# Kernel optimization log

Hardware: AMD Instinct MI355X
Metric: run time of the kernel (lower is better)

Reference implementation:

```python
import jax, jax.numpy as jnp
import numpy as np
from jax import lax

D_MODEL = 512
D_INNER = 1024   # expand=2
D_STATE = 16
D_CONV = 4
DT_RANK = 32     # ceil(d_model/16)
B = 32
T_LOW = 512
T_SKIP = 1024    # = 2*T_LOW (convtranspose k=4,s=2,p=1 doubles T)


def setup_inputs() -> dict:
    key = jax.random.key(0)
    ks = jax.random.split(key, 12)
    def rn(k, shape, scale):
        return jax.random.normal(k, shape, jnp.float32) * scale
    d, di = D_MODEL, D_INNER
    return {
        "x": rn(ks[0], (B, T_LOW, d), 1.0),
        "skip": rn(ks[1], (B, T_SKIP, d), 1.0),
        # ConvTranspose1d weight, torch layout (in, out, k)
        "up_w": rn(ks[2], (d, d, 4), (d * 4) ** -0.5),
        "up_b": jnp.zeros((d,), jnp.float32),
        # 1x1 fusion conv: (out, in=2d)
        "fus_w": rn(ks[3], (d, 2 * d), (2 * d) ** -0.5),
        "fus_b": jnp.zeros((d,), jnp.float32),
        "ln_g": jnp.ones((d,), jnp.float32),
        "ln_b": jnp.zeros((d,), jnp.float32),
        # Mamba params (1 layer)
        "in_w": rn(ks[4], (2 * di, d), d ** -0.5),
        "conv_w": rn(ks[5], (di, 1, D_CONV), D_CONV ** -0.5),  # depthwise
        "conv_b": jnp.zeros((di,), jnp.float32),
        "xproj_w": rn(ks[6], (DT_RANK + 2 * D_STATE, di), di ** -0.5),
        "dt_w": rn(ks[7], (di, DT_RANK), DT_RANK ** -0.5),
        "dt_b": jnp.log(jnp.expm1(jax.random.uniform(ks[8], (di,), jnp.float32, 1e-3, 0.1))),
        "A_log": jnp.log(jnp.tile(jnp.arange(1, D_STATE + 1, dtype=jnp.float32), (di, 1))),
        "Dp": jnp.ones((di,), jnp.float32),
        "out_w": rn(ks[9], (d, di), di ** -0.5),
    }


def reference(x, skip, up_w, up_b, fus_w, fus_b, ln_g, ln_b,
              in_w, conv_w, conv_b, xproj_w, dt_w, dt_b, A_log, Dp, out_w):
    # --- upsample: ConvTranspose1d(k=4, s=2, p=1): (B,T_low,d) -> (B,d,2*T_low)
    xc = x.transpose(0, 2, 1)                                  # (B, d, T_low)
    wt = jnp.swapaxes(jnp.flip(up_w, -1), 0, 1)                # (out, in, k)
    xu = lax.conv_general_dilated(
        xc, wt, window_strides=(1,), padding=[(2, 2)], lhs_dilation=(2,),
        dimension_numbers=("NCH", "OIH", "NCH")) + up_b[None, :, None]
    # T_up == T_skip by construction (no interpolate/slice needed)

    # --- skip fusion: concat on channels, 1x1 conv
    fused = jnp.concatenate([xu, skip.transpose(0, 2, 1)], axis=1)  # (B, 2d, T)
    fused = jnp.einsum("bct,oc->bto", fused, fus_w) + fus_b         # (B, T, d)

    # --- LayerNorm over d_model
    mu = fused.mean(-1, keepdims=True)
    var = fused.var(-1, keepdims=True)
    h = (fused - mu) * lax.rsqrt(var + 1e-5) * ln_g + ln_b

    # --- Mamba layer (mamba_ssm defaults) ---
    xz = h @ in_w.T                                            # (B, T, 2*Din)
    x_in, z = jnp.split(xz, 2, axis=-1)
    # causal depthwise conv1d (torch pads d_conv-1 both sides then truncates)
    xch = x_in.transpose(0, 2, 1)                              # (B, Din, T)
    xconv = lax.conv_general_dilated(
        xch, conv_w, window_strides=(1,), padding=[(D_CONV - 1, 0)],
        feature_group_count=D_INNER,
        dimension_numbers=("NCH", "OIH", "NCH")) + conv_b[None, :, None]
    xs = jax.nn.silu(xconv.transpose(0, 2, 1))                 # (B, T, Din)

    x_dbl = xs @ xproj_w.T                                     # (B, T, dt_rank+2S)
    dtr, Bm, Cm = jnp.split(x_dbl, [DT_RANK, DT_RANK + D_STATE], axis=-1)
    dt = jax.nn.softplus(dtr @ dt_w.T + dt_b)                  # (B, T, Din)
    A = -jnp.exp(A_log)                                        # (Din, S)

    def step(hst, ins):
        dt_t, b_t, c_t, x_t = ins                              # (B,Din),(B,S),(B,S),(B,Din)
        da = jnp.exp(dt_t[..., None] * A)                      # (B, Din, S)
        hst = hst * da + (dt_t * x_t)[..., None] * b_t[:, None, :]
        y = jnp.einsum("bds,bs->bd", hst, c_t)
        return hst, y

    h0 = jnp.zeros((xs.shape[0], D_INNER, D_STATE), xs.dtype)
    _, ys = lax.scan(step, h0, (dt.transpose(1, 0, 2), Bm.transpose(1, 0, 2),
                                Cm.transpose(1, 0, 2), xs.transpose(1, 0, 2)))
    y = ys.transpose(1, 0, 2) + xs * Dp                        # (B, T, Din)
    y = y * jax.nn.silu(z)
    out = y @ out_w.T                                          # (B, T, d)
    # dropout is identity in eval mode
    return out
```

## Files before the change

### kernel.cpp

```cpp
#include <hip/hip_runtime.h>
#include <hip/hip_bf16.h>
#include <math.h>

#define Bn    32
#define TLOW  512
#define Tt    1024
#define Dm    512
#define Din   1024
#define Dst   16
#define DTR   32
#define NC    16
#define Tc    64
#define L2E   1.44269504f

typedef unsigned short ushortt;
typedef __bf16 bf16x8 __attribute__((ext_vector_type(8)));
typedef unsigned short u16x8 __attribute__((ext_vector_type(8)));
typedef unsigned short u16x4 __attribute__((ext_vector_type(4)));
typedef float  f32x4  __attribute__((ext_vector_type(4)));

__device__ __forceinline__ ushortt f2b(float f) {
  union { float f; unsigned int u; } v; v.f = f;
  unsigned int r = v.u + 0x7FFFu + ((v.u >> 16) & 1u);
  return (ushortt)(r >> 16);
}
__device__ __forceinline__ float b2f(ushortt h) {
  union { unsigned int u; float f; } v; v.u = ((unsigned int)h) << 16;
  return v.f;
}
__device__ __forceinline__ ushortt f2h(float f) {
  _Float16 h = (_Float16)f; ushortt u; __builtin_memcpy(&u, &h, 2); return u;
}
__device__ __forceinline__ float h2f(ushortt u) {
  _Float16 h; __builtin_memcpy(&h, &u, 2); return (float)h;
}
__device__ __forceinline__ void gload16(const ushortt* g, ushortt* l) {
  __builtin_amdgcn_global_load_lds(
      (const __attribute__((address_space(1))) unsigned int*)g,
      (__attribute__((address_space(3))) unsigned int*)l, 16, 0, 0);
}
__device__ __forceinline__ float softplusf(float v) {
  float e = __builtin_amdgcn_exp2f(-fabsf(v) * L2E);
  return fmaxf(v, 0.f) + __logf(1.f + e);
}

template <typename OUT_T>
__global__ __launch_bounds__(256) void gemm_bf16(
    const ushortt* __restrict__ A0, const ushortt* __restrict__ A1,
    int lda, int ksplit,
    const ushortt* __restrict__ W,
    const float* __restrict__ bias,
    OUT_T* __restrict__ C, int ldc,
    int M, int N, int K, int bpad, int zA1, int zW, int zC)
{
  const int z = blockIdx.z;
  A1 += (size_t)z * zA1;
  W  += (size_t)z * zW;
  C  += (size_t)z * zC;

  __shared__ ushortt smem[8192];
  ushortt* As = smem;
  ushortt* Ws = smem + 4096;
  const int tid = threadIdx.x;
  const int m0 = blockIdx.y * 128;
  const int n0 = blockIdx.x * 128;
  const int lane = tid & 63;
  const int wv = tid >> 6;
  const int wm = wv & 1, wn = wv >> 1;
  const int arow0 = m0 + (bpad ? 2 * (m0 >> 9) : 0);

  f32x4 zz; zz[0] = 0.f; zz[1] = 0.f; zz[2] = 0.f; zz[3] = 0.f;
  f32x4 acc[4][4];
#pragma unroll
  for (int i = 0; i < 4; ++i)
#pragma unroll
    for (int j = 0; j < 4; ++j) acc[i][j] = zz;

  const int s0 = tid, s1 = tid + 256;
  const int r0 = s0 >> 2, c0 = (s0 & 3) * 8;
  const int r1 = s1 >> 2, c1 = (s1 & 3) * 8;

  for (int k0 = 0; k0 < K; k0 += 32) {
    const ushortt* Ab; int kc;
    if (k0 < ksplit) { Ab = A0; kc = k0; } else { Ab = A1; kc = k0 - ksplit; }
    gload16(Ab + (size_t)(arow0 + r0) * lda + kc + c0, As + s0 * 8);
    gload16(Ab + (size_t)(arow0 + r1) * lda + kc + c1, As + s1 * 8);
    gload16(W + (size_t)(n0 + r0) * K + k0 + c0, Ws + s0 * 8);
    gload16(W + (size_t)(n0 + r1) * K + k0 + c1, Ws + s1 * 8);
    __syncthreads();

    bf16x8 af[4], bfr[4];
    const int kk = (lane >> 4) * 8;
    const int ar = wm * 64 + (lane & 15);
    const int br = wn * 64 + (lane & 15);
#pragma unroll
    for (int i = 0; i < 4; ++i)
      af[i] = *(const bf16x8*)(As + (ar + i * 16) * 32 + kk);
#pragma unroll
    for (int i = 0; i < 4; ++i)
      bfr[i] = *(const bf16x8*)(Ws + (br + i * 16) * 32 + kk);
#pragma unroll
    for (int i = 0; i < 4; ++i)
#pragma unroll
      for (int j = 0; j < 4; ++j)
        acc[i][j] = __builtin_amdgcn_mfma_f32_16x16x32_bf16(af[i], bfr[j], acc[i][j], 0, 0, 0);
    __syncthreads();
  }

  const int crow = (lane >> 4) * 4;
  const int ccol = lane & 15;
  float bv[4];
#pragma unroll
  for (int j = 0; j < 4; ++j)
    bv[j] = bias ? bias[n0 + wn * 64 + j * 16 + ccol] : 0.f;

  if constexpr (sizeof(OUT_T) == 2) {
    for (int ph = 0; ph < 2; ++ph) {
      __syncthreads();
      if (wm == ph) {
#pragma unroll
        for (int i = 0; i < 4; ++i) {
          const int rl = i * 16 + crow;
#pragma unroll
          for (int j = 0; j < 4; ++j) {
            const int cl = wn * 64 + j * 16 + ccol;
#pragma unroll
            for (int ii = 0; ii < 4; ++ii) {
              const int r = rl + ii;
              const int cs = cl ^ (((r >> 2) & 7) << 4);
              smem[r * 128 + cs] = f2b(acc[i][j][ii] + bv[j]);
            }
          }
        }
      }
      __syncthreads();
      const int grb = m0 + ph * 64;
#pragma unroll
      for (int q = 0; q < 4; ++q) {
        const int g = tid + q * 256;
        const int r = g >> 4;
        const int cg = (g & 15) * 8;
        const int cs = cg ^ (((r >> 2) & 7) << 4);
        u16x8 v = *(const u16x8*)(smem + r * 128 + cs);
        *(u16x8*)((ushortt*)C + (size_t)(grb + r) * ldc + n0 + cg) = v;
      }
    }
  } else {
    float* smf = (float*)smem;
    for (int ph = 0; ph < 4; ++ph) {
      __syncthreads();
      if (wm == (ph >> 1)) {
#pragma unroll
        for (int io = 0; io < 2; ++io) {
          const int i = (ph & 1) * 2 + io;
          const int rl = i * 16 + crow - (ph & 1) * 32;
#pragma unroll
          for (int j = 0; j < 4; ++j) {
            const int cl = wn * 64 + j * 16 + ccol;
#pragma unroll
            for (int ii = 0; ii < 4; ++ii) {
              const int r = rl + ii;
              const int cs = cl ^ (((r >> 2) & 7) << 4);
              smf[r * 128 + cs] = acc[i][j][ii] + bv[j];
            }
          }
        }
      }
      __syncthreads();
      const int grb = m0 + ph * 32;
#pragma unroll
      for (int q = 0; q < 4; ++q) {
        const int g = tid + q * 256;
        const int r = g >> 5;
        const int cg = (g & 31) * 4;
        const int cs = cg ^ (((r >> 2) & 7) << 4);
        f32x4 v = *(const f32x4*)(smf + r * 128 + cs);
        *(f32x4*)((float*)C + (size_t)(grb + r) * ldc + n0 + cg) = v;
      }
    }
  }
}

__global__ __launch_bounds__(256) void wcvt_kernel(
    const float* __restrict__ a, ushortt* __restrict__ oa, int na,
    const float* __restrict__ b, ushortt* __restrict__ ob, int nb,
    const float* __restrict__ c, ushortt* __restrict__ oc, int nc) {
  int i = blockIdx.x * 256 + threadIdx.x;
  if (i < na) { oa[i] = f2b(a[i]); return; }
  i -= na;
  if (i < nb) { ob[i] = f2b(b[i]); return; }
  i -= nb;
  if (i < nc) oc[i] = f2b(c[i]);
}
__global__ __launch_bounds__(256) void wpad_kernel(
    const float* __restrict__ xpw, ushortt* __restrict__ oxp,
    const float* __restrict__ dtw, float* __restrict__ dtwT) {
  int i = blockIdx.x * 256 + threadIdx.x;
  if (i < 128 * 1024) {
    int row = i >> 10, col = i & 1023;
    oxp[i] = (row < 64) ? f2b(xpw[row * 1024 + col]) : (ushortt)0;
  } else {
    int j = i - 128 * 1024;
    int r = j >> 10, di = j & 1023;
    dtwT[j] = dtw[(size_t)di * DTR + r];
  }
}
__global__ __launch_bounds__(256) void wup_kernel(
    const float* __restrict__ upw, ushortt* __restrict__ wev,
    ushortt* __restrict__ wod) {
  int i = blockIdx.x * 256 + threadIdx.x;
  int ci = i >> 9, o = i & 511;
  const float4 w = ((const float4*)upw)[(size_t)ci * 512 + o];
  wev[(size_t)o * 1024 + ci]       = f2b(w.y);
  wev[(size_t)o * 1024 + 512 + ci] = f2b(w.w);
  wod[(size_t)o * 1024 + ci]       = f2b(w.z);
  wod[(size_t)o * 1024 + 512 + ci] = f2b(w.x);
}

__global__ __launch_bounds__(256) void actprep_kernel(
    const float* __restrict__ x, const float* __restrict__ skip,
    ushortt* __restrict__ xpad, ushortt* __restrict__ skb, int nxp4, int nt4) {
  int i = blockIdx.x * 256 + threadIdx.x;
  if (i >= nt4) return;
  if (i < nxp4) {
    int cg = i & 127;
    int rr = (i >> 7) % 514;
    int b = i / (514 * 128);
    float4 v = make_float4(0.f, 0.f, 0.f, 0.f);
    if (rr >= 1 && rr <= 512)
      v = ((const float4*)x)[((size_t)b * TLOW + rr - 1) * 128 + cg];
    u16x4 o; o[0] = f2b(v.x); o[1] = f2b(v.y); o[2] = f2b(v.z); o[3] = f2b(v.w);
    *(u16x4*)(xpad + (size_t)i * 4) = o;
  } else {
    int j = i - nxp4;
    float4 v = ((const float4*)skip)[j];
    u16x4 o; o[0] = f2b(v.x); o[1] = f2b(v.y); o[2] = f2b(v.z); o[3] = f2b(v.w);
    *(u16x4*)(skb + (size_t)j * 4) = o;
  }
}

__global__ __launch_bounds__(256) void ln_kernel(
    const float* __restrict__ fin, const float* __restrict__ g,
    const float* __restrict__ bta, ushortt* __restrict__ out)
{
  const int row = blockIdx.x;
  const int tid = threadIdx.x;
  const float* p = fin + (size_t)row * Dm;
  float v0 = p[tid], v1 = p[tid + 256];
  float s = v0 + v1;
  float q = v0 * v0 + v1 * v1;
#pragma unroll
  for (int off = 32; off > 0; off >>= 1) {
    s += __shfl_down(s, off, 64);
    q += __shfl_down(q, off, 64);
  }
  __shared__ float ss[4], qq[4];
  int wid = tid >> 6;
  if ((tid & 63) == 0) { ss[wid] = s; qq[wid] = q; }
  __syncthreads();
  float sum = ss[0] + ss[1] + ss[2] + ss[3];
  float sq  = qq[0] + qq[1] + qq[2] + qq[3];
  float mu  = sum * (1.f / 512.f);
  float var = sq * (1.f / 512.f) - mu * mu;
  float rs  = rsqrtf(var + 1e-5f);
  out[(size_t)row * Dm + tid]       = f2b((v0 - mu) * rs * g[tid] + bta[tid]);
  out[(size_t)row * Dm + tid + 256] = f2b((v1 - mu) * rs * g[tid + 256] + bta[tid + 256]);
}

__global__ __launch_bounds__(256) void dwconv_kernel(
    const ushortt* __restrict__ xz, const float* __restrict__ cw,
    const float* __restrict__ cb, ushortt* __restrict__ xs)
{
  const int g = blockIdx.x * 256 + threadIdx.x;
  const int di0 = (g & 127) << 3;
  const int bt0 = (g >> 7) << 3;
  const int t0 = bt0 & (Tt - 1);
  const ushortt* rowp = xz + (size_t)bt0 * (2 * Din) + di0;

  u16x8 rw[11];
#pragma unroll
  for (int k = 0; k < 11; ++k) {
    if (t0 - 3 + k >= 0) {
      rw[k] = *(const u16x8*)(rowp + (ptrdiff_t)(k - 3) * (2 * Din));
    } else {
      u16x8 zv = {0, 0, 0, 0, 0, 0, 0, 0};
      rw[k] = zv;
    }
  }
  float4 w4[8]; float cbv[8];
#pragma unroll
  for (int j = 0; j < 8; ++j) {
    w4[j] = ((const float4*)cw)[di0 + j];
    cbv[j] = cb[di0 + j];
  }
  ushortt* op = xs + (size_t)bt0 * Din + di0;
#pragma unroll
  for (int o = 0; o < 8; ++o) {
    u16x8 ov;
#pragma unroll
    for (int j = 0; j < 8; ++j) {
      float a = cbv[j];
      a = fmaf(w4[j].x, b2f(rw[o][j]), a);
      a = fmaf(w4[j].y, b2f(rw[o + 1][j]), a);
      a = fmaf(w4[j].z, b2f(rw[o + 2][j]), a);
      a = fmaf(w4[j].w, b2f(rw[o + 3][j]), a);
      float sg = 1.f / (1.f + __expf(-a));
      ov[j] = f2b(a * sg);
    }
    *(u16x8*)(op + (size_t)o * Din) = ov;
  }
}

__global__ __launch_bounds__(256) void dt_kernel(
    const float* __restrict__ xdbl,
    const float* __restrict__ dtwT,
    const float* __restrict__ dtb,
    ushortt* __restrict__ dt16)
{
  const int gid = blockIdx.x * 256 + threadIdx.x;
  const int di0 = (gid & 127) << 3;
  const int row0 = (gid >> 7) << 2;
  float a0[8], a1[8], a2[8], a3[8];
#pragma unroll
  for (int j = 0; j < 8; ++j) {
    float b = dtb[di0 + j];
    a0[j] = b; a1[j] = b; a2[j] = b; a3[j] = b;
  }
  const float* d0 = xdbl + (size_t)row0 * 128;
#pragma unroll
  for (int r = 0; r < DTR; ++r) {
    float u0 = d0[r], u1 = d0[128 + r], u2 = d0[256 + r], u3 = d0[384 + r];
    const float* wp = dtwT + r * 1024 + di0;
#pragma unroll
    for (int j = 0; j < 8; ++j) {
      float w = wp[j];
      a0[j] = fmaf(u0, w, a0[j]);
      a1[j] = fmaf(u1, w, a1[j]);
      a2[j] = fmaf(u2, w, a2[j]);
      a3[j] = fmaf(u3, w, a3[j]);
    }
  }
  u16x8 o0, o1, o2, o3;
#pragma unroll
  for (int j = 0; j < 8; ++j) {
    o0[j] = f2h(softplusf(a0[j]));
    o1[j] = f2h(softplusf(a1[j]));
    o2[j] = f2h(softplusf(a2[j]));
    o3[j] = f2h(softplusf(a3[j]));
  }
  ushortt* yp = dt16 + (size_t)row0 * 1024 + di0;
  *(u16x8*)(yp)        = o0;
  *(u16x8*)(yp + 1024) = o1;
  *(u16x8*)(yp + 2048) = o2;
  *(u16x8*)(yp + 3072) = o3;
}

__global__ __launch_bounds__(256) void scan_p1(
    const float* __restrict__ xdbl,
    const ushortt* __restrict__ dt16,
    const ushortt* __restrict__ xs,
    const float* __restrict__ Alog,
    float* __restrict__ pq)
{
  const int di = blockIdx.x * 256 + threadIdx.x;
  const int b  = blockIdx.y;
  const int c  = blockIdx.z;
  const float a1l = -__expf(Alog[(size_t)di * Dst]) * L2E;

  float Q[Dst];
#pragma unroll
  for (int s = 0; s < Dst; ++s) Q[s] = 0.f;
  float dtsum = 0.f;

  const size_t rowb = (size_t)b * Tt + (size_t)c * Tc;
  const float* dr = xdbl + rowb * 128 + 32;
  const ushortt* dtp = dt16 + rowb * Din + di;
  const ushortt* xsp = xs + rowb * Din + di;

  for (int t = 0; t < Tc; ++t) {
    float dt = h2f(dtp[0]);
    float xv = b2f(xsp[0]);
    float c1 = dt * xv;
    float r = __builtin_amdgcn_exp2f(dt * a1l);
    dtsum += dt;
    float rp = r;
#pragma unroll
    for (int s = 0; s < Dst; ++s) {
      Q[s] = fmaf(Q[s], rp, c1 * dr[s]);
      rp *= r;
    }
    dr += 128; dtp += Din; xsp += Din;
  }
  float e1 = __builtin_amdgcn_exp2f(dtsum * a1l);
  float ep = e1;
  float* o = pq + ((size_t)(b * NC + c) * 32) * Din + di;
#pragma unroll
  for (int s = 0; s < Dst; ++s) {
    o[(size_t)s * Din] = ep;
    ep *= e1;
    o[(size_t)(16 + s) * Din] = Q[s];
  }
}

__global__ __launch_bounds__(256) void scan_p3(
    const float* __restrict__ xdbl,
    const ushortt* __restrict__ dt16,
    const ushortt* __restrict__ xs,
    const ushortt* __restrict__ xz,
    const float* __restrict__ Alog, const float* __restrict__ Dpp,
    const float* __restrict__ pq,
    ushortt* __restrict__ y)
{
  const int di = blockIdx.x * 256 + threadIdx.x;
  const int b  = blockIdx.y;
  const int c  = blockIdx.z;
  const float a1l = -__expf(Alog[(size_t)di * Dst]) * L2E;
  const float dp = Dpp[di];

  float h[Dst];
#pragma unroll
  for (int s = 0; s < Dst; ++s) h[s] = 0.f;
  for (int cc = 0; cc < c; ++cc) {
    const float* o = pq + ((size_t)(b * NC + cc) * 32) * Din + di;
#pragma unroll
    for (int s = 0; s < Dst; ++s)
      h[s] = fmaf(h[s], o[(size_t)s * Din], o[(size_t)(16 + s) * Din]);
  }

  const size_t rowb = (size_t)b * Tt + (size_t)c * Tc;
  const float* dr = xdbl + rowb * 128;
  const ushortt* dtp = dt16 + rowb * Din + di;
  const ushortt* xsp = xs + rowb * Din + di;
  const ushortt* zp  = xz + rowb * (2 * Din) + Din + di;
  ushortt* yp = y + rowb * Din + di;

  for (int t = 0; t < Tc; ++t) {
    float dt = h2f(dtp[0]);
    float xv = b2f(xsp[0]);
    float c1 = dt * xv;
    float r = __builtin_amdgcn_exp2f(dt * a1l);
    float rp = r;
    float yacc = 0.f;
#pragma unroll
    for (int s = 0; s < Dst; ++s) {
      h[s] = fmaf(h[s], rp, c1 * dr[32 + s]);
      yacc = fmaf(h[s], dr[48 + s], yacc);
      rp *= r;
    }
    float zv = b2f(zp[0]);
    float sig = 1.f / (1.f + __expf(-zv));
    yp[0] = f2b((yacc + xv * dp) * (zv * sig));
    dr += 128; dtp += Din; xsp += Din; zp += 2 * Din; yp += Din;
  }
}

extern "C" void kernel_launch(void* const* d_in, const int* in_sizes, int n_in,
                              void* d_out, int out_size, void* d_ws, size_t ws_size,
                              hipStream_t stream) {
  const float* x      = (const float*)d_in[0];
  const float* skip   = (const float*)d_in[1];
  const float* up_w   = (const float*)d_in[2];
  const float* up_b   = (const float*)d_in[3];
  const float* fus_w  = (const float*)d_in[4];
  const float* fus_b  = (const float*)d_in[5];
  const float* ln_g   = (const float*)d_in[6];
  const float* ln_b   = (const float*)d_in[7];
  const float* in_w   = (const float*)d_in[8];
  const float* conv_w = (const float*)d_in[9];
  const float* conv_b = (const float*)d_in[10];
  const float* xproj_w= (const float*)d_in[11];
  const float* dt_w   = (const float*)d_in[12];
  const float* dt_b   = (const float*)d_in[13];
  const float* A_log  = (const float*)d_in[14];
  const float* Dp     = (const float*)d_in[15];
  const float* out_w  = (const float*)d_in[16];

  char* ws = (char*)d_ws;
  ushortt* Wfus = (ushortt*)ws;                 ws += (size_t)512 * 1024 * 2;
  ushortt* Win  = (ushortt*)ws;                 ws += (size_t)2048 * 512 * 2;
  ushortt* Wout = (ushortt*)ws;                 ws += (size_t)512 * 1024 * 2;
  ushortt* Wxp  = (ushortt*)ws;                 ws += (size_t)128 * 1024 * 2;
  ushortt* Wev  = (ushortt*)ws;                 ws += (size_t)512 * 1024 * 2;
  ushortt* Wod  = (ushortt*)ws;                 ws += (size_t)512 * 1024 * 2;
  float*   dtwT = (float*)ws;                   ws += (size_t)32 * 1024 * 4;
  const size_t wbytes = (size_t)(ws - (char*)d_ws);

  const size_t per_b = 526336ull
      + (size_t)Tt * (1024 + 2048 + 2048 + 4096 + 2048 + 512) + 2097152ull;
  int Bc = Bn;
  while (Bc > 1 && wbytes + (size_t)Bc * per_b > ws_size) Bc >>= 1;
  const size_t NR = (size_t)Bc * Tt;

  ushortt* xpad = (ushortt*)ws;                 ws += (size_t)Bc * 526336;
  ushortt* skb  = (ushortt*)ws;                 ws += NR * 1024;
  ushortt* xu   = (ushortt*)ws;                 ws += NR * 2048;
  float*   fused= (float*)ws;                   ws += NR * 2048;
  ushortt* xzb  = (ushortt*)ws;                 ws += NR * 4096;
  ushortt* xsb  = (ushortt*)ws;                 ws += NR * 2048;
  float*   xdbl = (float*)ws;                   ws += NR * 512;
  float*   pq   = (float*)ws;                   ws += (size_t)Bc * NC * 32 * Din * 4;
  ushortt* hbuf = skb;
  ushortt* yb   = xu;
  ushortt* dt16 = (ushortt*)fused;

  {
    const int na = 512 * 1024, nb = 2048 * 512, ncc = 512 * 1024;
    wcvt_kernel<<<(na + nb + ncc + 255) / 256, 256, 0, stream>>>(
        fus_w, Wfus, na, in_w, Win, nb, out_w, Wout, ncc);
    wpad_kernel<<<(128 * 1024 + 32 * 1024) / 256, 256, 0, stream>>>(
        xproj_w, Wxp, dt_w, dtwT);
    wup_kernel<<<(512 * 512) / 256, 256, 0, stream>>>(up_w, Wev, Wod);
  }

  for (int b0 = 0; b0 < Bn; b0 += Bc) {
    const float* xk    = x    + (size_t)b0 * TLOW * Dm;
    const float* skipk = skip + (size_t)b0 * Tt * Dm;
    float*       outk  = (float*)d_out + (size_t)b0 * Tt * Dm;
    const int Mu = Bc * TLOW;

    {
      const int nxp4 = Bc * 514 * 128;
      const int nt4 = nxp4 + (int)(NR * 128);
      actprep_kernel<<<(nt4 + 255) / 256, 256, 0, stream>>>(xk, skipk, xpad, skb, nxp4, nt4);
    }

    gemm_bf16<ushortt><<<dim3(4, Mu / 128, 2), 256, 0, stream>>>(
        xpad + 512, xpad, 512, 512, Wev, up_b, xu, 1024,
        Mu, 512, 1024, 1, 1024, 512 * 1024, 512);

    gemm_bf16<float><<<dim3(4, (int)(NR / 128)), 256, 0, stream>>>(
        xu, skb, 512, 512, Wfus, fus_b, fused, 512,
        (int)NR, 512, 1024, 0, 0, 0, 0);

    ln_kernel<<<(int)NR, 256, 0, stream>>>(fused, ln_g, ln_b, hbuf);

    gemm_bf16<ushortt><<<dim3(16, (int)(NR / 128)), 256, 0, stream>>>(
        hbuf, hbuf, 512, 512, Win, nullptr, xzb, 2048,
        (int)NR, 2048, 512, 0, 0, 0, 0);

    dwconv_kernel<<<(int)(NR / 16), 256, 0, stream>>>(xzb, conv_w, conv_b, xsb);

    gemm_bf16<float><<<dim3(1, (int)(NR / 128)), 256, 0, stream>>>(
        xsb, xsb, 1024, 1024, Wxp, nullptr, xdbl, 128,
        (int)NR, 128, 1024, 0, 0, 0, 0);

    dt_kernel<<<(int)(NR / 8), 256, 0, stream>>>(xdbl, dtwT, dt_b, dt16);

    scan_p1<<<dim3(Din / 256, Bc, NC - 1), 256, 0, stream>>>(
        xdbl, dt16, xsb, A_log, pq);
    scan_p3<<<dim3(Din / 256, Bc, NC), 256, 0, stream>>>(
        xdbl, dt16, xsb, xzb, A_log, Dp, pq, yb);

    gemm_bf16<float><<<dim3(4, (int)(NR / 128)), 256, 0, stream>>>(
        yb, yb, 1024, 1024, Wout, nullptr, outk, 512,
        (int)NR, 512, 1024, 0, 0, 0, 0);
  }
}
```

Before: 755.2 us.

## Fold upsample weights into fusion conv and add LDS swizzle with workgroup remap

Precomputes a combined weight (fusion weight times the even/odd transposed-conv weights) plus a folded bias, so the upsample GEMM and the fusion GEMM become one GEMM with K=1536 reading xpad and skip directly. This removes the xu intermediate write and read and one GEMM launch per chunk. It also XOR-swizzles the LDS tile columns to reduce bank conflicts and remaps workgroup IDs across 8 groups for cache locality. The trade-off is more FLOPs per output row (K grows from 1024 to 1536) and a double bf16 rounding of the combined weights.

```diff
diff --git a/kernel.cpp b/kernel.cpp
--- a/kernel.cpp
+++ b/kernel.cpp
@@ -47,23 +47,30 @@
 template <typename OUT_T>
 __global__ __launch_bounds__(256) void gemm_bf16(
     const ushortt* __restrict__ A0, const ushortt* __restrict__ A1,
-    int lda, int ksplit,
+    const ushortt* __restrict__ A2,
+    int lda, int lda2, int ks1, int ks2,
     const ushortt* __restrict__ W,
     const float* __restrict__ bias,
     OUT_T* __restrict__ C, int ldc,
-    int M, int N, int K, int bpad, int zA1, int zW, int zC)
+    int M, int N, int K, int bpad,
+    int zA1, int zA2, int zW, int zC)
 {
   const int z = blockIdx.z;
   A1 += (size_t)z * zA1;
+  A2 += (size_t)z * zA2;
   W  += (size_t)z * zW;
   C  += (size_t)z * zC;
+
+  const int nwg = gridDim.x * gridDim.y;
+  int w = blockIdx.y * gridDim.x + blockIdx.x;
+  if (!(nwg & 7)) w = (w & 7) * (nwg >> 3) + (w >> 3);
+  const int m0 = (w / gridDim.x) * 128;
+  const int n0 = (w % gridDim.x) * 128;
 
   __shared__ ushortt smem[8192];
   ushortt* As = smem;
   ushortt* Ws = smem + 4096;
   const int tid = threadIdx.x;
-  const int m0 = blockIdx.y * 128;
-  const int n0 = blockIdx.x * 128;
   const int lane = tid & 63;
   const int wv = tid >> 6;
   const int wm = wv & 1, wn = wv >> 1;
@@ -77,28 +84,31 @@
     for (int j = 0; j < 4; ++j) acc[i][j] = zz;
 
   const int s0 = tid, s1 = tid + 256;
-  const int r0 = s0 >> 2, c0 = (s0 & 3) * 8;
-  const int r1 = s1 >> 2, c1 = (s1 & 3) * 8;
+  const int r0 = s0 >> 2, c0 = (((s0 & 3) ^ ((r0 >> 1) & 3)) * 8);
+  const int r1 = s1 >> 2, c1 = (((s1 & 3) ^ ((r1 >> 1) & 3)) * 8);
 
   for (int k0 = 0; k0 < K; k0 += 32) {
-    const ushortt* Ab; int kc;
-    if (k0 < ksplit) { Ab = A0; kc = k0; } else { Ab = A1; kc = k0 - ksplit; }
-    gload16(Ab + (size_t)(arow0 + r0) * lda + kc + c0, As + s0 * 8);
-    gload16(Ab + (size_t)(arow0 + r1) * lda + kc + c1, As + s1 * 8);
+    const ushortt* Ab; int kc, ldax, rbase;
+    if (k0 < ks1)      { Ab = A0; kc = k0;       ldax = lda;  rbase = arow0; }
+    else if (k0 < ks2) { Ab = A1; kc = k0 - ks1; ldax = lda;  rbase = arow0; }
+    else               { Ab = A2; kc = k0 - ks2; ldax = lda2; rbase = m0; }
+    gload16(Ab + (size_t)(rbase + r0) * ldax + kc + c0, As + s0 * 8);
+    gload16(Ab + (size_t)(rbase + r1) * ldax + kc + c1, As + s1 * 8);
     gload16(W + (size_t)(n0 + r0) * K + k0 + c0, Ws + s0 * 8);
     gload16(W + (size_t)(n0 + r1) * K + k0 + c1, Ws + s1 * 8);
     __syncthreads();
 
     bf16x8 af[4], bfr[4];
-    const int kk = (lane >> 4) * 8;
     const int ar = wm * 64 + (lane & 15);
     const int br = wn * 64 + (lane & 15);
+    const int kxA = (((lane >> 4) ^ ((ar >> 1) & 3)) * 8);
+    const int kxB = (((lane >> 4) ^ ((br >> 1) & 3)) * 8);
 #pragma unroll
     for (int i = 0; i < 4; ++i)
-      af[i] = *(const bf16x8*)(As + (ar + i * 16) * 32 + kk);
+      af[i] = *(const bf16x8*)(As + (ar + i * 16) * 32 + kxA);
 #pragma unroll
     for (int i = 0; i < 4; ++i)
-      bfr[i] = *(const bf16x8*)(Ws + (br + i * 16) * 32 + kk);
+      bfr[i] = *(const bf16x8*)(Ws + (br + i * 16) * 32 + kxB);
 #pragma unroll
     for (int i = 0; i < 4; ++i)
 #pragma unroll
@@ -194,27 +204,51 @@
 }
 __global__ __launch_bounds__(256) void wpad_kernel(
     const float* __restrict__ xpw, ushortt* __restrict__ oxp,
-    const float* __restrict__ dtw, float* __restrict__ dtwT) {
+    const float* __restrict__ dtw, float* __restrict__ dtwT,
+    const float* __restrict__ fusw, ushortt* __restrict__ wcomb) {
   int i = blockIdx.x * 256 + threadIdx.x;
   if (i < 128 * 1024) {
     int row = i >> 10, col = i & 1023;
     oxp[i] = (row < 64) ? f2b(xpw[row * 1024 + col]) : (ushortt)0;
-  } else {
-    int j = i - 128 * 1024;
-    int r = j >> 10, di = j & 1023;
-    dtwT[j] = dtw[(size_t)di * DTR + r];
+    return;
+  }
+  i -= 128 * 1024;
+  if (i < 32 * 1024) {
+    int r = i >> 10, di = i & 1023;
+    dtwT[i] = dtw[(size_t)di * DTR + r];
+    return;
+  }
+  i -= 32 * 1024;
+  if (i < 512 * 512) {
+    int d = i >> 9, col = i & 511;
+    ushortt v = f2b(fusw[(size_t)d * 1024 + 512 + col]);
+    wcomb[(size_t)d * 1536 + 1024 + col] = v;
+    wcomb[(size_t)512 * 1536 + d * 1536 + 1024 + col] = v;
   }
 }
 __global__ __launch_bounds__(256) void wup_kernel(
-    const float* __restrict__ upw, ushortt* __restrict__ wev,
-    ushortt* __restrict__ wod) {
+    const float* __restrict__ upw, ushortt* __restrict__ wevT) {
   int i = blockIdx.x * 256 + threadIdx.x;
   int ci = i >> 9, o = i & 511;
   const float4 w = ((const float4*)upw)[(size_t)ci * 512 + o];
-  wev[(size_t)o * 1024 + ci]       = f2b(w.y);
-  wev[(size_t)o * 1024 + 512 + ci] = f2b(w.w);
-  wod[(size_t)o * 1024 + ci]       = f2b(w.z);
-  wod[(size_t)o * 1024 + 512 + ci] = f2b(w.x);
+  ushortt* wodT = wevT + 1024 * 512;
+  wevT[(size_t)ci * 512 + o]         = f2b(w.y);
+  wevT[(size_t)(512 + ci) * 512 + o] = f2b(w.w);
+  wodT[(size_t)ci * 512 + o]         = f2b(w.z);
+  wodT[(size_t)(512 + ci) * 512 + o] = f2b(w.x);
+}
+__global__ __launch_bounds__(256) void fbias_kernel(
+    const float* __restrict__ fusw, const float* __restrict__ fusb,
+    const float* __restrict__ upb, float* __restrict__ fb) {
+  int d = blockIdx.x * 256 + threadIdx.x;
+  float acc = fusb[d];
+  const float4* wr = (const float4*)(fusw + (size_t)d * 1024);
+  for (int o = 0; o < 128; ++o) {
+    float4 wv = wr[o];
+    float4 bv = ((const float4*)upb)[o];
+    acc += wv.x * bv.x + wv.y * bv.y + wv.z * bv.z + wv.w * bv.w;
+  }
+  fb[d] = acc;
 }
 
 __global__ __launch_bounds__(256) void actprep_kernel(
@@ -480,9 +514,10 @@
   ushortt* Win  = (ushortt*)ws;                 ws += (size_t)2048 * 512 * 2;
   ushortt* Wout = (ushortt*)ws;                 ws += (size_t)512 * 1024 * 2;
   ushortt* Wxp  = (ushortt*)ws;                 ws += (size_t)128 * 1024 * 2;
-  ushortt* Wev  = (ushortt*)ws;                 ws += (size_t)512 * 1024 * 2;
-  ushortt* Wod  = (ushortt*)ws;                 ws += (size_t)512 * 1024 * 2;
+  ushortt* WevT = (ushortt*)ws;                 ws += (size_t)2 * 1024 * 512 * 2;
+  ushortt* Wcomb= (ushortt*)ws;                 ws += (size_t)2 * 512 * 1536 * 2;
   float*   dtwT = (float*)ws;                   ws += (size_t)32 * 1024 * 4;
+  float*   fbias= (float*)ws;                   ws += (size_t)512 * 4;
   const size_t wbytes = (size_t)(ws - (char*)d_ws);
 
   const size_t per_b = 526336ull
@@ -507,16 +542,19 @@
     const int na = 512 * 1024, nb = 2048 * 512, ncc = 512 * 1024;
     wcvt_kernel<<<(na + nb + ncc + 255) / 256, 256, 0, stream>>>(
         fus_w, Wfus, na, in_w, Win, nb, out_w, Wout, ncc);
-    wpad_kernel<<<(128 * 1024 + 32 * 1024) / 256, 256, 0, stream>>>(
-        xproj_w, Wxp, dt_w, dtwT);
-    wup_kernel<<<(512 * 512) / 256, 256, 0, stream>>>(up_w, Wev, Wod);
+    wpad_kernel<<<(128 * 1024 + 32 * 1024 + 512 * 512) / 256, 256, 0, stream>>>(
+        xproj_w, Wxp, dt_w, dtwT, fus_w, Wcomb);
+    wup_kernel<<<(512 * 512) / 256, 256, 0, stream>>>(up_w, WevT);
+    fbias_kernel<<<2, 256, 0, stream>>>(fus_w, fus_b, up_b, fbias);
+    gemm_bf16<ushortt><<<dim3(8, 4, 2), 256, 0, stream>>>(
+        Wfus, Wfus, nullptr, 1024, 0, 512, 512, WevT, nullptr,
+        Wcomb, 1536, 512, 1024, 512, 0, 0, 0, 1024 * 512, 512 * 1536);
   }
 
   for (int b0 = 0; b0 < Bn; b0 += Bc) {
     const float* xk    = x    + (size_t)b0 * TLOW * Dm;
     const float* skipk = skip + (size_t)b0 * Tt * Dm;
     float*       outk  = (float*)d_out + (size_t)b0 * Tt * Dm;
-    const int Mu = Bc * TLOW;
 
     {
       const int nxp4 = Bc * 514 * 128;
@@ -524,25 +562,22 @@
       actprep_kernel<<<(nt4 + 255) / 256, 256, 0, stream>>>(xk, skipk, xpad, skb, nxp4, nt4);
     }
 
-    gemm_bf16<ushortt><<<dim3(4, Mu / 128, 2), 256, 0, stream>>>(
-        xpad + 512, xpad, 512, 512, Wev, up_b, xu, 1024,
-        Mu, 512, 1024, 1, 1024, 512 * 1024, 512);
-
-    gemm_bf16<float><<<dim3(4, (int)(NR / 128)), 256, 0, stream>>>(
-        xu, skb, 512, 512, Wfus, fus_b, fused, 512,
-        (int)NR, 512, 1024, 0, 0, 0, 0);
+    gemm_bf16<float><<<dim3(4, (int)(NR / 256), 2), 256, 0, stream>>>(
+        xpad + 512, xpad, skb, 512, 1024, 512, 1024, Wcomb, fbias,
+        fused, 1024, (int)(NR / 2), 512, 1536, 1,
+        1024, 512, 512 * 1536, 512);
 
     ln_kernel<<<(int)NR, 256, 0, stream>>>(fused, ln_g, ln_b, hbuf);
 
     gemm_bf16<ushortt><<<dim3(16, (int)(NR / 128)), 256, 0, stream>>>(
-        hbuf, hbuf, 512, 512, Win, nullptr, xzb, 2048,
-        (int)NR, 2048, 512, 0, 0, 0, 0);
+        hbuf, hbuf, nullptr, 512, 0, 512, 512, Win, nullptr, xzb, 2048,
+        (int)NR, 2048, 512, 0, 0, 0, 0, 0);
 
     dwconv_kernel<<<(int)(NR / 16), 256, 0, stream>>>(xzb, conv_w, conv_b, xsb);
 
     gemm_bf16<float><<<dim3(1, (int)(NR / 128)), 256, 0, stream>>>(
-        xsb, xsb, 1024, 1024, Wxp, nullptr, xdbl, 128,
-        (int)NR, 128, 1024, 0, 0, 0, 0);
+        xsb, xsb, nullptr, 1024, 0, 1024, 1024, Wxp, nullptr, xdbl, 128,
+        (int)NR, 128, 1024, 0, 0, 0, 0, 0);
 
     dt_kernel<<<(int)(NR / 8), 256, 0, stream>>>(xdbl, dtwT, dt_b, dt16);
 
@@ -552,7 +587,7 @@
         xdbl, dt16, xsb, xzb, A_log, Dp, pq, yb);
 
     gemm_bf16<float><<<dim3(4, (int)(NR / 128)), 256, 0, stream>>>(
-        yb, yb, 1024, 1024, Wout, nullptr, outk, 512,
-        (int)NR, 512, 1024, 0, 0, 0, 0);
-  }
-}
+        yb, yb, nullptr, 1024, 0, 1024, 1024, Wout, nullptr, outk, 512,
+        (int)NR, 512, 1024, 0, 0, 0, 0, 0);
+  }
+}
```

Measured after the change: 708.4 us. 1.07x faster.
